# Optimization experiments

Hardware: AMD Instinct MI355X
Metric: run time of the kernel (lower is better)

Reference implementation:

```python
import jax, jax.numpy as jnp
import numpy as np

N_V, M, K, C, H, F, CO = 100000, 25000, 48, 64, 4, 256, 64


def setup_inputs() -> dict:
    key = jax.random.key(0)
    ks = jax.random.split(key, 16)
    w = lambda k, shape: (jax.random.normal(k, shape, jnp.float32) * 0.05)
    voxel_features = jax.random.normal(ks[0], (N_V, C), jnp.float32)
    voxel_coords = jax.random.uniform(ks[1], (N_V, 3), jnp.float32) * 70.0 - 35.0
    query_coords = jax.random.uniform(ks[2], (M, 3), jnp.float32) * 70.0 - 35.0
    key_indices = jax.random.randint(ks[3], (M, K), 0, N_V, jnp.int32)
    key_mask = jax.random.uniform(ks[4], (M, K)) < 0.3
    key_mask = key_mask.at[:, 0].set(False)  # guarantee >=1 valid key per query
    zeros = lambda n: jnp.zeros((n,), jnp.float32)
    ones = lambda n: jnp.ones((n,), jnp.float32)
    return dict(
        voxel_features=voxel_features, voxel_coords=voxel_coords,
        query_coords=query_coords, key_indices=key_indices, key_mask=key_mask,
        q_pos_w=w(ks[5], (C, 3)), q_pos_b=zeros(C),
        k_pos_w=w(ks[6], (C, 3)), k_pos_b=zeros(C),
        in_proj_w=w(ks[7], (3 * C, C)), in_proj_b=zeros(3 * C),
        out_proj_w=w(ks[8], (C, C)), out_proj_b=zeros(C),
        lin1_w=w(ks[9], (F, C)), lin1_b=zeros(F),
        lin2_w=w(ks[10], (C, F)), lin2_b=zeros(C),
        norm_g=ones(C), norm_b=zeros(C), norm_m=zeros(C), norm_v=ones(C),
        out_w=w(ks[11], (CO, C)), out_b=zeros(CO),
        bn2_g=ones(CO), bn2_b=zeros(CO), bn2_m=zeros(CO), bn2_v=ones(CO),
    )


def reference(voxel_features, voxel_coords, query_coords, key_indices, key_mask,
              q_pos_w, q_pos_b, k_pos_w, k_pos_b, in_proj_w, in_proj_b,
              out_proj_w, out_proj_b, lin1_w, lin1_b, lin2_w, lin2_b,
              norm_g, norm_b, norm_m, norm_v, out_w, out_b,
              bn2_g, bn2_b, bn2_m, bn2_v):
    m, k = key_indices.shape
    c = voxel_features.shape[1]
    h = H
    d = c // h
    # grouping_operation: gather per-query key features/coords  (M,K,C)/(M,K,3)
    key_feats = voxel_features[key_indices]
    rel = voxel_coords[key_indices] - query_coords[:, None, :]  # relative coords
    # k_pos_proj: Conv1d(3->C, kernel 1) + ReLU == pointwise linear
    key_pos = jax.nn.relu(jnp.einsum('mkt,ct->mkc', rel, k_pos_w) + k_pos_b)
    k_in = key_feats + key_pos                      # (M,K,C)
    # q_pos_proj: Linear(3->C) + ReLU
    q_in = jax.nn.relu(query_coords @ q_pos_w.T + q_pos_b)  # (M,C)
    # nn.MultiheadAttention, query len 1, batch = M, keys = K
    wq, wk, wv = jnp.split(in_proj_w, 3, axis=0)
    bq, bk, bv = jnp.split(in_proj_b, 3)
    q = ((q_in @ wq.T + bq) * (d ** -0.5)).reshape(m, h, d)
    kk = (k_in @ wk.T + bk).reshape(m, k, h, d)
    vv = (k_in @ wv.T + bv).reshape(m, k, h, d)
    s = jnp.einsum('mhd,mkhd->mhk', q, kk)
    s = jnp.where(key_mask[:, None, :], -1e9, s)    # key_padding_mask
    a = jax.nn.softmax(s, axis=-1)
    o = jnp.einsum('mhk,mkhd->mhd', a, vv).reshape(m, c)
    attend = o @ out_proj_w.T + out_proj_b          # (M,C)
    # FFN residual (dropouts are identity in eval)
    ff = jax.nn.relu(attend @ lin1_w.T + lin1_b) @ lin2_w.T + lin2_b
    x = attend + ff
    # BatchNorm1d (eval)
    x = (x - norm_m) / jnp.sqrt(norm_v + 1e-5) * norm_g + norm_b
    # output_layer: Linear -> BN -> ReLU
    y = x @ out_w.T + out_b
    y = (y - bn2_m) / jnp.sqrt(bn2_v + 1e-5) * bn2_g + bn2_b
    return jax.nn.relu(y)
```

## Files before the change

### kernel.cpp

```cpp
#include <hip/hip_runtime.h>
#include <math.h>

#define CC 64
#define KK 48
#define HH 4

typedef __attribute__((ext_vector_type(8))) short s16x8;
typedef __attribute__((ext_vector_type(4))) short s16x4;
typedef __attribute__((ext_vector_type(4))) float f32x4;

#define QW_OFF_U16 57344
#define CASTB 1024

#define WAVEFENCE() asm volatile("s_waitcnt lgkmcnt(0)" ::: "memory")

__device__ __forceinline__ unsigned short f2bf(float f) {
  return (unsigned short)((__float_as_uint(f) + 0x8000u) >> 16);
}
__device__ __forceinline__ float bf2f(unsigned short h) {
  return __uint_as_float(((unsigned)h) << 16);
}

__global__ __launch_bounds__(256) void setup_kernel(
    const float* __restrict__ ipw, const float* __restrict__ opw,
    const float* __restrict__ l1w, const float* __restrict__ l2w,
    const float* __restrict__ ow,
    const float* __restrict__ ng, const float* __restrict__ nb,
    const float* __restrict__ nm, const float* __restrict__ nv,
    const float* __restrict__ b2g, const float* __restrict__ b2b,
    const float* __restrict__ b2m, const float* __restrict__ b2v,
    const unsigned char* __restrict__ km,
    const float* __restrict__ vf, const float* __restrict__ vcoord,
    const float* __restrict__ qcoord, const float* __restrict__ qpw,
    const float* __restrict__ qpb, const float* __restrict__ ipb,
    float* __restrict__ ws,
    unsigned short* __restrict__ vfb, float4* __restrict__ vc4,
    unsigned short* __restrict__ qw_out, int M, int NV)
{
  unsigned short* wsu = (unsigned short*)ws;
  const int b = blockIdx.x;

  if (b < 210) {
    if (b == 209) {
      int any = 0;
      for (int i = threadIdx.x; i < 4096; i += 256)
        if ((i & 3) && km[i]) any = 1;
      __shared__ int sb;
      if (threadIdx.x == 0) sb = 0;
      __syncthreads();
      if (any) atomicOr(&sb, 1);
      __syncthreads();
      if (threadIdx.x == 0) ((int*)ws)[26880] = sb;
      return;
    }
    int e = b * 256 + threadIdx.x;
    if (e < 4096)        wsu[e] = f2bf(ipw[e]);
    else if (e < 8192)  { int i = e - 4096; int h = i >> 10, c = (i >> 4) & 63, d = i & 15;
                          wsu[e] = f2bf(ipw[(size_t)(64 + h * 16 + d) * 64 + c]); }
    else if (e < 12288)  wsu[e] = f2bf(ipw[e]);
    else if (e < 16384)  wsu[e] = f2bf(opw[e - 12288]);
    else if (e < 32768)  wsu[e] = f2bf(l1w[e - 16384]);
    else if (e < 49152)  wsu[e] = f2bf(l2w[e - 32768]);
    else if (e < 53248)  wsu[e] = f2bf(ow[e - 49152]);
    else if (e < 53312) { int c = e - 53248; float s = ng[c] / sqrtf(nv[c] + 1e-5f);
                          ws[26624 + c] = s; ws[26624 + 64 + c] = nb[c] - nm[c] * s; }
    else if (e < 53376) { int c = e - 53312; float s = b2g[c] / sqrtf(b2v[c] + 1e-5f);
                          ws[26752 + c] = s; ws[26752 + 64 + c] = b2b[c] - b2m[c] * s; }
    return;
  }

  if (b < 210 + CASTB) {
    const int i0 = (b - 210) * 256 + threadIdx.x;
    const int stride = CASTB * 256;
    for (int i = i0; i < NV * 16; i += stride) {
      const float4 v = *(const float4*)(vf + (size_t)i * 4);
      s16x4 p; p[0] = (short)f2bf(v.x); p[1] = (short)f2bf(v.y);
      p[2] = (short)f2bf(v.z); p[3] = (short)f2bf(v.w);
      *(s16x4*)(vfb + (size_t)i * 4) = p;
    }
    for (int i = i0; i < NV; i += stride)
      vc4[i] = make_float4(vcoord[i * 3], vcoord[i * 3 + 1], vcoord[i * 3 + 2], 0.f);
    return;
  }

  {
    __shared__ __align__(16) unsigned short xa[4][1024];
    __shared__ float qc[4][48];
    const int w = threadIdx.x >> 6, l = threadIdx.x & 63;
    const int col = l & 15, lg = l >> 4;
    const int r0 = (b - 210 - CASTB) * 64 + w * 16;

    if (l < 48) {
      int gi = r0 * 3 + l;
      qc[w][l] = (gi < M * 3) ? qcoord[gi] : 0.f;
    }
    const int c0 = col * 4;
    const float4 wA = *(const float4*)(qpw + c0 * 3);
    const float4 wB = *(const float4*)(qpw + c0 * 3 + 4);
    const float4 wC = *(const float4*)(qpw + c0 * 3 + 8);
    const float4 bq4 = *(const float4*)(qpb + c0);
    __syncthreads();

    #pragma unroll
    for (int i = 0; i < 4; ++i) {
      const int row = i * 4 + lg;
      const float x = qc[w][row * 3 + 0], y = qc[w][row * 3 + 1], z = qc[w][row * 3 + 2];
      s16x4 p;
      p[0] = (short)f2bf(fmaxf(wA.x * x + wA.y * y + wA.z * z + bq4.x, 0.f));
      p[1] = (short)f2bf(fmaxf(wA.w * x + wB.x * y + wB.y * z + bq4.y, 0.f));
      p[2] = (short)f2bf(fmaxf(wB.z * x + wB.w * y + wC.x * z + bq4.z, 0.f));
      p[3] = (short)f2bf(fmaxf(wC.y * x + wC.z * y + wC.w * z + bq4.w, 0.f));
      *(s16x4*)&xa[w][(row * 64 + c0) ^ ((row & 7) << 3)] = p;
    }
    __syncthreads();

    {
      s16x8 af0 = *(const s16x8*)&xa[w][(col * 64 + 0 + lg * 8) ^ ((col & 7) << 3)];
      s16x8 af1 = *(const s16x8*)&xa[w][(col * 64 + 32 + lg * 8) ^ ((col & 7) << 3)];
      f32x4 qv[4];
      #pragma unroll
      for (int nt = 0; nt < 4; ++nt) {
        f32x4 acc = {0.f, 0.f, 0.f, 0.f};
        #pragma unroll
        for (int kst = 0; kst < 2; ++kst) {
          const float* wr = ipw + (size_t)(nt * 16 + col) * 64 + kst * 32 + lg * 8;
          const float4 w0 = *(const float4*)wr;
          const float4 w1 = *(const float4*)(wr + 4);
          s16x8 bf;
          bf[0] = (short)f2bf(w0.x); bf[1] = (short)f2bf(w0.y);
          bf[2] = (short)f2bf(w0.z); bf[3] = (short)f2bf(w0.w);
          bf[4] = (short)f2bf(w1.x); bf[5] = (short)f2bf(w1.y);
          bf[6] = (short)f2bf(w1.z); bf[7] = (short)f2bf(w1.w);
          acc = __builtin_amdgcn_mfma_f32_16x16x32_bf16(kst == 0 ? af0 : af1, bf, acc, 0, 0, 0);
        }
        qv[nt] = acc;
      }
      __syncthreads();
      #pragma unroll
      for (int nt = 0; nt < 4; ++nt) {
        const int n = nt * 16 + col;
        const float bb = ipb[n];
        #pragma unroll
        for (int r = 0; r < 4; ++r) {
          const int row = lg * 4 + r;
          xa[w][(row * 64 + n) ^ ((row & 7) << 3)] = f2bf((qv[nt][r] + bb) * 0.25f);
        }
      }
    }
    __syncthreads();

    #pragma unroll
    for (int h = 0; h < HH; ++h) {
      s16x8 a = {0, 0, 0, 0, 0, 0, 0, 0};
      if (lg < 2)
        a = *(const s16x8*)&xa[w][(col * 64 + h * 16 + lg * 8) ^ ((col & 7) << 3)];
      #pragma unroll
      for (int nt = 0; nt < 4; ++nt) {
        const int n = nt * 16 + col;
        s16x8 bf = {0, 0, 0, 0, 0, 0, 0, 0};
        if (lg < 2) {
          #pragma unroll
          for (int j = 0; j < 8; ++j)
            ((unsigned short*)&bf)[j] = f2bf(ipw[(size_t)(64 + h * 16 + lg * 8 + j) * 64 + n]);
        }
        f32x4 acc = {0.f, 0.f, 0.f, 0.f};
        acc = __builtin_amdgcn_mfma_f32_16x16x32_bf16(a, bf, acc, 0, 0, 0);
        #pragma unroll
        for (int r = 0; r < 4; ++r) {
          const int m = lg * 4 + r;
          if (r0 + m < M)
            qw_out[(size_t)(r0 + m) * 256 + h * 64 + n] = f2bf(acc[r]);
        }
      }
    }
  }
}

__global__ __launch_bounds__(256, 4) void attn_hot(
    const unsigned short* __restrict__ vfb, const float4* __restrict__ vc4,
    const float* __restrict__ qcoord, const int* __restrict__ kidx,
    const unsigned char* __restrict__ km8, const int* __restrict__ km32,
    const int* __restrict__ maskfmt,
    const float* __restrict__ kpw, const float* __restrict__ kpb,
    const float* __restrict__ ipb,
    const unsigned short* __restrict__ wv_bf,
    const unsigned short* __restrict__ qw_pre,
    float* __restrict__ out, int M)
{
  __shared__ __align__(16) unsigned short shq[4][3456];
  __shared__ __align__(16) unsigned short wvl[4096];
  const int w = threadIdx.x >> 6, l = threadIdx.x & 63;
  const int col = l & 15, lg = l >> 4;
  int m = blockIdx.x * 4 + w;
  if (m >= M) m = M - 1;
  unsigned short* sh = shq[w];
  float* relf = (float*)(sh + 3072);
  const int is_u8 = *maskfmt;

  #pragma unroll
  for (int i = 0; i < 2; ++i) {
    const int ch = threadIdx.x * 2 + i;
    const int n = ch >> 3, g = ch & 7;
    const s16x8 v = *(const s16x8*)(wv_bf + n * 64 + g * 8);
    *(s16x8*)&wvl[n * 64 + ((g ^ (n & 7)) << 3)] = v;
  }

  const float qx = qcoord[m * 3 + 0], qy = qcoord[m * 3 + 1], qz = qcoord[m * 3 + 2];
  const int c0 = col * 4;
  const float4 kwA = *(const float4*)(kpw + c0 * 3);
  const float4 kwB = *(const float4*)(kpw + c0 * 3 + 4);
  const float4 kwC = *(const float4*)(kpw + c0 * 3 + 8);
  const float4 kbv = *(const float4*)(kpb + c0);

  const s16x8 qb0 = *(const s16x8*)(qw_pre + (size_t)m * 256 + (col & 3) * 64 + 0 + lg * 8);
  const s16x8 qb1 = *(const s16x8*)(qw_pre + (size_t)m * 256 + (col & 3) * 64 + 32 + lg * 8);

  unsigned char msk = 0;
  if (l < KK) {
    const int idx = kidx[m * KK + l];
    msk = is_u8 ? km8[m * KK + l] : (unsigned char)(km32[m * KK + l] != 0);
    const float4 vc = vc4[idx];
    float4 rr;
    rr.x = vc.x - qx; rr.y = vc.y - qy; rr.z = vc.z - qz;
    rr.w = __int_as_float(idx);
    *(float4*)(relf + l * 4) = rr;
  }
  const unsigned long long bm = __ballot(l < KK && msk);
  __syncthreads();

  #pragma unroll
  for (int half = 0; half < 2; ++half) {
    float4 ra[6]; s16x4 va[6];
    #pragma unroll
    for (int j = 0; j < 6; ++j) {
      const int k = half * 24 + j * 4 + lg;
      ra[j] = *(const float4*)(relf + k * 4);
      va[j] = *(const s16x4*)(vfb + (size_t)__float_as_int(ra[j].w) * 64 + c0);
    }
    #pragma unroll
    for (int j = 0; j < 6; ++j) {
      const int k = half * 24 + j * 4 + lg;
      const float p0 = fmaxf(kwA.x * ra[j].x + kwA.y * ra[j].y + kwA.z * ra[j].z + kbv.x, 0.f);
      const float p1 = fmaxf(kwA.w * ra[j].x + kwB.x * ra[j].y + kwB.y * ra[j].z + kbv.y, 0.f);
      const float p2 = fmaxf(kwB.z * ra[j].x + kwB.w * ra[j].y + kwC.x * ra[j].z + kbv.z, 0.f);
      const float p3 = fmaxf(kwC.y * ra[j].x + kwC.z * ra[j].y + kwC.w * ra[j].z + kbv.w, 0.f);
      s16x4 p;
      p[0] = (short)f2bf(bf2f((unsigned short)va[j][0]) + p0);
      p[1] = (short)f2bf(bf2f((unsigned short)va[j][1]) + p1);
      p[2] = (short)f2bf(bf2f((unsigned short)va[j][2]) + p2);
      p[3] = (short)f2bf(bf2f((unsigned short)va[j][3]) + p3);
      *(s16x4*)&sh[(k * 64 + c0) ^ ((k & 7) << 3)] = p;
    }
  }
  WAVEFENCE();

  s16x8 af[3][2];
  #pragma unroll
  for (int mt = 0; mt < 3; ++mt)
    #pragma unroll
    for (int kst = 0; kst < 2; ++kst) {
      const int row = mt * 16 + col;
      af[mt][kst] = *(const s16x8*)&sh[(row * 64 + kst * 32 + lg * 8) ^ ((row & 7) << 3)];
    }
  f32x4 sc[3];
  sc[0] = sc[1] = sc[2] = (f32x4){0.f, 0.f, 0.f, 0.f};
  __builtin_amdgcn_s_setprio(1);
  #pragma unroll
  for (int mt = 0; mt < 3; ++mt) {
    sc[mt] = __builtin_amdgcn_mfma_f32_16x16x32_bf16(af[mt][0], qb0, sc[mt], 0, 0, 0);
    sc[mt] = __builtin_amdgcn_mfma_f32_16x16x32_bf16(af[mt][1], qb1, sc[mt], 0, 0, 0);
  }
  __builtin_amdgcn_s_setprio(0);

  float sv[12];
  {
    float mx = -INFINITY;
    #pragma unroll
    for (int mt = 0; mt < 3; ++mt)
      #pragma unroll
      for (int r = 0; r < 4; ++r) {
        const int key = mt * 16 + lg * 4 + r;
        float v = sc[mt][r];
        if ((bm >> key) & 1ull) v = -1e30f;
        sv[mt * 4 + r] = v;
        mx = fmaxf(mx, v);
      }
    mx = fmaxf(mx, __shfl_xor(mx, 16, 64));
    mx = fmaxf(mx, __shfl_xor(mx, 32, 64));
    float sum = 0.f;
    #pragma unroll
    for (int i = 0; i < 12; ++i) { float e = __expf(sv[i] - mx); sv[i] = e; sum += e; }
    sum += __shfl_xor(sum, 16, 64);
    sum += __shfl_xor(sum, 32, 64);
    const float inv = 1.f / sum;
    #pragma unroll
    for (int i = 0; i < 12; ++i) sv[i] *= inv;
  }
  if (col < HH) {
    #pragma unroll
    for (int mt = 0; mt < 3; ++mt)
      #pragma unroll
      for (int r = 0; r < 4; ++r)
        relf[(mt * 16 + lg * 4 + r) * 4 + col] = sv[mt * 4 + r];
  }
  WAVEFENCE();

  f32x4 vva[4][3];
  __builtin_amdgcn_s_setprio(1);
  #pragma unroll
  for (int nt = 0; nt < 4; ++nt) {
    const int n = nt * 16 + col;
    vva[nt][0] = vva[nt][1] = vva[nt][2] = (f32x4){0.f, 0.f, 0.f, 0.f};
    #pragma unroll
    for (int kst = 0; kst < 2; ++kst) {
      const s16x8 b = *(const s16x8*)&wvl[(n * 64 + kst * 32 + lg * 8) ^ ((n & 7) << 3)];
      vva[nt][0] = __builtin_amdgcn_mfma_f32_16x16x32_bf16(af[0][kst], b, vva[nt][0], 0, 0, 0);
      vva[nt][1] = __builtin_amdgcn_mfma_f32_16x16x32_bf16(af[1][kst], b, vva[nt][1], 0, 0, 0);
      vva[nt][2] = __builtin_amdgcn_mfma_f32_16x16x32_bf16(af[2][kst], b, vva[nt][2], 0, 0, 0);
    }
  }
  __builtin_amdgcn_s_setprio(0);
  float op[4] = {0.f, 0.f, 0.f, 0.f};
  #pragma unroll
  for (int mt = 0; mt < 3; ++mt)
    #pragma unroll
    for (int r = 0; r < 4; ++r) {
      const float4 a4 = *(const float4*)(relf + (mt * 16 + lg * 4 + r) * 4);
      op[0] += a4.x * vva[0][mt][r];
      op[1] += a4.y * vva[1][mt][r];
      op[2] += a4.z * vva[2][mt][r];
      op[3] += a4.w * vva[3][mt][r];
    }
  #pragma unroll
  for (int nt = 0; nt < 4; ++nt) {
    op[nt] += __shfl_xor(op[nt], 16, 64);
    op[nt] += __shfl_xor(op[nt], 32, 64);
  }
  {
    float oo = (lg == 0) ? op[0] : (lg == 1) ? op[1] : (lg == 2) ? op[2] : op[3];
    oo += ipb[2 * CC + lg * 16 + col];
    out[(size_t)m * CC + lg * 16 + col] = oo;
  }
}

__global__ __launch_bounds__(256) void prep_kernel(
    const float* __restrict__ ipw, const float* __restrict__ opw,
    const float* __restrict__ l1w, const float* __restrict__ l2w,
    const float* __restrict__ ow,
    const float* __restrict__ ng, const float* __restrict__ nb,
    const float* __restrict__ nm, const float* __restrict__ nv,
    const float* __restrict__ b2g, const float* __restrict__ b2b,
    const float* __restrict__ b2m, const float* __restrict__ b2v,
    const unsigned char* __restrict__ km,
    float* __restrict__ ws)
{
  unsigned short* wsu = (unsigned short*)ws;
  if (blockIdx.x == 209) {
    int any = 0;
    for (int i = threadIdx.x; i < 4096; i += 256)
      if ((i & 3) && km[i]) any = 1;
    __shared__ int sb;
    if (threadIdx.x == 0) sb = 0;
    __syncthreads();
    if (any) atomicOr(&sb, 1);
    __syncthreads();
    if (threadIdx.x == 0) ((int*)ws)[26880] = sb;
    return;
  }
  int e = blockIdx.x * 256 + threadIdx.x;
  if (e < 4096)        wsu[e] = f2bf(ipw[e]);
  else if (e < 8192)  { int i = e - 4096; int h = i >> 10, c = (i >> 4) & 63, d = i & 15;
                        wsu[e] = f2bf(ipw[(size_t)(64 + h * 16 + d) * 64 + c]); }
  else if (e < 12288)  wsu[e] = f2bf(ipw[e]);
  else if (e < 16384)  wsu[e] = f2bf(opw[e - 12288]);
  else if (e < 32768)  wsu[e] = f2bf(l1w[e - 16384]);
  else if (e < 49152)  wsu[e] = f2bf(l2w[e - 32768]);
  else if (e < 53248)  wsu[e] = f2bf(ow[e - 49152]);
  else if (e < 53312) { int c = e - 53248; float s = ng[c] / sqrtf(nv[c] + 1e-5f);
                        ws[26624 + c] = s; ws[26624 + 64 + c] = nb[c] - nm[c] * s; }
  else if (e < 53376) { int c = e - 53312; float s = b2g[c] / sqrtf(b2v[c] + 1e-5f);
                        ws[26752 + c] = s; ws[26752 + 64 + c] = b2b[c] - b2m[c] * s; }
}

__global__ __launch_bounds__(256, 4) void attn_fallback(
    const float* __restrict__ vfeat, const float* __restrict__ vcoord,
    const float* __restrict__ qcoord, const int* __restrict__ kidx,
    const unsigned char* __restrict__ km8, const int* __restrict__ km32,
    const int* __restrict__ maskfmt,
    const float* __restrict__ qpw, const float* __restrict__ qpb,
    const float* __restrict__ kpw, const float* __restrict__ kpb,
    const float* __restrict__ ipb,
    const unsigned short* __restrict__ wq_bf,
    const unsigned short* __restrict__ wk2T_bf,
    const unsigned short* __restrict__ wv_bf,
    float* __restrict__ out, int M)
{
  __shared__ __align__(16) unsigned short shq[4][3776];
  __shared__ __align__(16) unsigned short wvl[4096];
  const int w = threadIdx.x >> 6, l = threadIdx.x & 63;
  const int col = l & 15, lg = l >> 4;
  int m = blockIdx.x * 4 + w;
  if (m >= M) m = M - 1;
  unsigned short* sh = shq[w];
  const int is_u8 = *maskfmt;
  float* relf = (float*)sh + 1696;

  #pragma unroll
  for (int i = 0; i < 2; ++i) {
    const int ch = threadIdx.x * 2 + i;
    const int n = ch >> 3, g = ch & 7;
    const s16x8 v = *(const s16x8*)(wv_bf + n * 64 + g * 8);
    *(s16x8*)&wvl[n * 64 + ((g ^ (n & 7)) << 3)] = v;
  }

  const float qx = qcoord[m * 3 + 0], qy = qcoord[m * 3 + 1], qz = qcoord[m * 3 + 2];
  const int c0 = col * 4;
  const float4 kwA = *(const float4*)(kpw + c0 * 3);
  const float4 kwB = *(const float4*)(kpw + c0 * 3 + 4);
  const float4 kwC = *(const float4*)(kpw + c0 * 3 + 8);
  const float4 kbv = *(const float4*)(kpb + c0);

  {
    float v = qpw[l * 3 + 0] * qx + qpw[l * 3 + 1] * qy + qpw[l * 3 + 2] * qz + qpb[l];
    sh[3328 + l] = f2bf(fmaxf(v, 0.f));
  }
  unsigned char msk = 0;
  if (l < KK) {
    int idx = kidx[m * KK + l];
    msk = is_u8 ? km8[m * KK + l] : (unsigned char)(km32[m * KK + l] != 0);
    relf[l * 4 + 0] = vcoord[idx * 3 + 0] - qx;
    relf[l * 4 + 1] = vcoord[idx * 3 + 1] - qy;
    relf[l * 4 + 2] = vcoord[idx * 3 + 2] - qz;
    relf[l * 4 + 3] = __int_as_float(idx);
  }
  const unsigned long long bm = __ballot(l < KK && msk);
  __syncthreads();

  {
    f32x4 qacc[4];
    #pragma unroll
    for (int nt = 0; nt < 4; ++nt) qacc[nt] = (f32x4){0.f, 0.f, 0.f, 0.f};
    #pragma unroll
    for (int kst = 0; kst < 2; ++kst) {
      const s16x8 a = *(const s16x8*)&sh[3328 + kst * 32 + lg * 8];
      #pragma unroll
      for (int nt = 0; nt < 4; ++nt) {
        const s16x8 b = *(const s16x8*)(wq_bf + (nt * 16 + col) * 64 + kst * 32 + lg * 8);
        qacc[nt] = __builtin_amdgcn_mfma_f32_16x16x32_bf16(a, b, qacc[nt], 0, 0, 0);
      }
    }
    __syncthreads();
    if (lg == 0) {
      #pragma unroll
      for (int nt = 0; nt < 4; ++nt)
        sh[3328 + nt * 16 + col] = f2bf((qacc[nt][0] + ipb[nt * 16 + col]) * 0.25f);
    }
    __syncthreads();
    f32x4 wacc[4];
    #pragma unroll
    for (int nt = 0; nt < 4; ++nt) wacc[nt] = (f32x4){0.f, 0.f, 0.f, 0.f};
    #pragma unroll
    for (int kst = 0; kst < 2; ++kst) {
      const int hblk = kst * 2 + (lg >> 1);
      s16x8 a = {0, 0, 0, 0, 0, 0, 0, 0};
      if (col == hblk) a = *(const s16x8*)&sh[3328 + kst * 32 + lg * 8];
      #pragma unroll
      for (int nt = 0; nt < 4; ++nt) {
        const s16x8 b = *(const s16x8*)(wk2T_bf + hblk * 1024 + (nt * 16 + col) * 16 + (lg & 1) * 8);
        wacc[nt] = __builtin_amdgcn_mfma_f32_16x16x32_bf16(a, b, wacc[nt], 0, 0, 0);
      }
    }
    if (lg == 0) {
      #pragma unroll
      for (int nt = 0; nt < 4; ++nt)
        #pragma unroll
        for (int r = 0; r < 4; ++r)
          sh[3072 + r * 64 + nt * 16 + col] = f2bf(wacc[nt][r]);
    }
  }

  #pragma unroll
  for (int half = 0; half < 2; ++half) {
    float4 ra[6], va[6];
    #pragma unroll
    for (int j = 0; j < 6; ++j) {
      const int k = half * 24 + j * 4 + lg;
      ra[j] = *(const float4*)(relf + k * 4);
      va[j] = *(const float4*)(vfeat + (size_t)__float_as_int(ra[j].w) * 64 + c0);
    }
    #pragma unroll
    for (int j = 0; j < 6; ++j) {
      const int k = half * 24 + j * 4 + lg;
      const float p0 = fmaxf(kwA.x * ra[j].x + kwA.y * ra[j].y + kwA.z * ra[j].z + kbv.x, 0.f);
      const float p1 = fmaxf(kwA.w * ra[j].x + kwB.x * ra[j].y + kwB.y * ra[j].z + kbv.y, 0.f);
// ... 104 lines not shown
  const unsigned short* l1_bf  = wsu + 16384;
  const unsigned short* l2_bf  = wsu + 32768;
  const unsigned short* ow_bf  = wsu + 49152;

  #pragma unroll
  for (int i = 0; i < 4; ++i) {
    int row = i * 4 + lg, cb = col * 4;
    float4 v = make_float4(0.f, 0.f, 0.f, 0.f);
    if (r0 + row < M) v = *(const float4*)(&inout[(size_t)(r0 + row) * 64 + cb]);
    s16x4 p; p[0] = (short)f2bf(v.x); p[1] = (short)f2bf(v.y);
    p[2] = (short)f2bf(v.z); p[3] = (short)f2bf(v.w);
    *(s16x4*)&XH[(row * 64 + cb) ^ ((row & 7) << 3)] = p;
  }

  s16x8 afa[2];
  #pragma unroll
  for (int kst = 0; kst < 2; ++kst)
    afa[kst] = *(const s16x8*)&XH[(col * 64 + kst * 32 + lg * 8) ^ ((col & 7) << 3)];
  f32x4 att[4];
  #pragma unroll
  for (int nt = 0; nt < 4; ++nt) {
    f32x4 acc = {0.f, 0.f, 0.f, 0.f};
    #pragma unroll
    for (int kst = 0; kst < 2; ++kst) {
      const s16x8 b = *(const s16x8*)&opw_bf[(nt * 16 + col) * 64 + kst * 32 + lg * 8];
      acc = __builtin_amdgcn_mfma_f32_16x16x32_bf16(afa[kst], b, acc, 0, 0, 0);
    }
    float bias = opb[nt * 16 + col];
    #pragma unroll
    for (int r = 0; r < 4; ++r) {
      acc[r] += bias;
      int row = lg * 4 + r;
      XB[(row * 64 + nt * 16 + col) ^ ((row & 7) << 3)] = (short)f2bf(acc[r]);
    }
    att[nt] = acc;
  }

  s16x8 afb[2];
  #pragma unroll
  for (int kst = 0; kst < 2; ++kst)
    afb[kst] = *(const s16x8*)&XB[(col * 64 + kst * 32 + lg * 8) ^ ((col & 7) << 3)];
  #pragma unroll
  for (int nt = 0; nt < 16; ++nt) {
    f32x4 acc = {0.f, 0.f, 0.f, 0.f};
    #pragma unroll
    for (int kst = 0; kst < 2; ++kst) {
      const s16x8 b = *(const s16x8*)&l1_bf[(nt * 16 + col) * 64 + kst * 32 + lg * 8];
      acc = __builtin_amdgcn_mfma_f32_16x16x32_bf16(afb[kst], b, acc, 0, 0, 0);
    }
    float bias = l1b[nt * 16 + col];
    #pragma unroll
    for (int r = 0; r < 4; ++r) {
      float h = fmaxf(acc[r] + bias, 0.f);
      int row = lg * 4 + r;
      XH[(row * 256 + nt * 16 + col) ^ ((row & 7) << 3)] = (short)f2bf(h);
    }
  }

  s16x8 afh[8];
  #pragma unroll
  for (int kst = 0; kst < 8; ++kst)
    afh[kst] = *(const s16x8*)&XH[(col * 256 + kst * 32 + lg * 8) ^ ((col & 7) << 3)];
  #pragma unroll
  for (int nt = 0; nt < 4; ++nt) {
    f32x4 acc = {0.f, 0.f, 0.f, 0.f};
    #pragma unroll
    for (int kst = 0; kst < 8; ++kst) {
      const s16x8 b = *(const s16x8*)&l2_bf[(nt * 16 + col) * 256 + kst * 32 + lg * 8];
      acc = __builtin_amdgcn_mfma_f32_16x16x32_bf16(afh[kst], b, acc, 0, 0, 0);
    }
    int nc = nt * 16 + col;
    float bias = l2b[nc], sN = nrm[nc], tN = nrm[64 + nc];
    #pragma unroll
    for (int r = 0; r < 4; ++r) {
      float x = (att[nt][r] + acc[r] + bias) * sN + tN;
      int row = lg * 4 + r;
      XB[(row * 64 + nc) ^ ((row & 7) << 3)] = (short)f2bf(x);
    }
  }

  s16x8 afx[2];
  #pragma unroll
  for (int kst = 0; kst < 2; ++kst)
    afx[kst] = *(const s16x8*)&XB[(col * 64 + kst * 32 + lg * 8) ^ ((col & 7) << 3)];
  #pragma unroll
  for (int nt = 0; nt < 4; ++nt) {
    f32x4 acc = {0.f, 0.f, 0.f, 0.f};
    #pragma unroll
    for (int kst = 0; kst < 2; ++kst) {
      const s16x8 b = *(const s16x8*)&ow_bf[(nt * 16 + col) * 64 + kst * 32 + lg * 8];
      acc = __builtin_amdgcn_mfma_f32_16x16x32_bf16(afx[kst], b, acc, 0, 0, 0);
    }
    int nc = nt * 16 + col;
    float bias = ob[nc], sB = bn2[nc], tB = bn2[64 + nc];
    #pragma unroll
    for (int r = 0; r < 4; ++r) {
      float y = fmaxf((acc[r] + bias) * sB + tB, 0.f);
      int row = lg * 4 + r;
      if (r0 + row < M) inout[(size_t)(r0 + row) * 64 + nc] = y;
    }
  }
}

extern "C" void kernel_launch(void* const* d_in, const int* in_sizes, int n_in,
                              void* d_out, int out_size, void* d_ws, size_t ws_size,
                              hipStream_t stream) {
  const float* vfeat  = (const float*)d_in[0];
  const float* vcoord = (const float*)d_in[1];
  const float* qcoord = (const float*)d_in[2];
  const int*   kidx   = (const int*)d_in[3];
  const unsigned char* km8  = (const unsigned char*)d_in[4];
  const int*           km32 = (const int*)d_in[4];
  const float* qpw = (const float*)d_in[5];
  const float* qpb = (const float*)d_in[6];
  const float* kpw = (const float*)d_in[7];
  const float* kpb = (const float*)d_in[8];
  const float* ipw = (const float*)d_in[9];
  const float* ipb = (const float*)d_in[10];
  const float* opw = (const float*)d_in[11];
  const float* opb = (const float*)d_in[12];
  const float* l1w = (const float*)d_in[13];
  const float* l1b = (const float*)d_in[14];
  const float* l2w = (const float*)d_in[15];
  const float* l2b = (const float*)d_in[16];
  const float* ng  = (const float*)d_in[17];
  const float* nb  = (const float*)d_in[18];
  const float* nm  = (const float*)d_in[19];
  const float* nv  = (const float*)d_in[20];
  const float* ow  = (const float*)d_in[21];
  const float* ob  = (const float*)d_in[22];
  const float* b2g = (const float*)d_in[23];
  const float* b2b = (const float*)d_in[24];
  const float* b2m = (const float*)d_in[25];
  const float* b2v = (const float*)d_in[26];

  const int M  = in_sizes[2] / 3;
  const int NV = in_sizes[0] / 64;
  float* ws  = (float*)d_ws;
  float* out = (float*)d_out;
  unsigned short* wsu = (unsigned short*)ws;
  const int* flag = (const int*)ws + 26880;

  const size_t need = (size_t)114688 + (size_t)M * 512 + (size_t)NV * 128 + (size_t)NV * 16;
  const int hot = (ws_size >= need) ? 1 : 0;
  unsigned short* qw  = wsu + QW_OFF_U16;
  unsigned short* vfb = wsu + QW_OFF_U16 + (size_t)M * 256;
  float4* vc4 = (float4*)(wsu + QW_OFF_U16 + (size_t)M * 256 + (size_t)NV * 64);

  if (hot) {
    const int qblocks = (M + 63) / 64;
    setup_kernel<<<210 + CASTB + qblocks, 256, 0, stream>>>(
        ipw, opw, l1w, l2w, ow, ng, nb, nm, nv, b2g, b2b, b2m, b2v, km8,
        vfeat, vcoord, qcoord, qpw, qpb, ipb, ws, vfb, vc4, qw, M, NV);
    attn_hot<<<(M + 3) / 4, 256, 0, stream>>>(vfb, vc4, qcoord, kidx,
                                              km8, km32, flag, kpw, kpb, ipb,
                                              wsu + 8192, qw, out, M);
  } else {
    prep_kernel<<<210, 256, 0, stream>>>(ipw, opw, l1w, l2w, ow,
                                         ng, nb, nm, nv, b2g, b2b, b2m, b2v, km8, ws);
    attn_fallback<<<(M + 3) / 4, 256, 0, stream>>>(vfeat, vcoord, qcoord, kidx,
                                                   km8, km32, flag,
                                                   qpw, qpb, kpw, kpb, ipb,
                                                   wsu, wsu + 4096, wsu + 8192, out, M);
  }
  chain_kernel<<<(M + 63) / 64, 256, 0, stream>>>(out, wsu, opb, l1b, l2b, ob,
                                                  ws + 26624, ws + 26752, M);
}
```

Baseline: 93.80 us.

## Fuse attention with output projection, FFN and BN chain in one kernel

The attention kernel now processes 16 queries per block (4 per wave, looped) and then runs the out-projection, FFN, residual, batchnorm and output layer on those 16 rows in shared memory using MFMA. This removes the separate chain kernel launch and the fp32 round trip of the attention output through global memory. The setup kernel also stages the Wq and transposed Wk weights into LDS as bf16 once per block instead of converting them from global memory per lane. The costs are fewer blocks with serialized per-query work, extra block-wide barriers, and bf16 rounding of intermediate activations.

```diff
diff --git a/kernel.cpp b/kernel.cpp
--- a/kernel.cpp
+++ b/kernel.cpp
@@ -84,12 +84,19 @@
   }
 
   {
+    __shared__ __align__(16) unsigned short wql[4096];
+    __shared__ __align__(16) unsigned short wkTl[4096];
     __shared__ __align__(16) unsigned short xa[4][1024];
     __shared__ float qc[4][48];
     const int w = threadIdx.x >> 6, l = threadIdx.x & 63;
     const int col = l & 15, lg = l >> 4;
     const int r0 = (b - 210 - CASTB) * 64 + w * 16;
 
+    for (int i = threadIdx.x; i < 4096; i += 256) {
+      const int r = i >> 6, d = i & 63;
+      wql[i ^ ((r & 7) << 3)] = f2bf(ipw[i]);
+      wkTl[(d * 64 + r) ^ ((d & 7) << 3)] = f2bf(ipw[4096 + i]);
+    }
     if (l < 48) {
       int gi = r0 * 3 + l;
       qc[w][l] = (gi < M * 3) ? qcoord[gi] : 0.f;
@@ -120,19 +127,12 @@
       f32x4 qv[4];
       #pragma unroll
       for (int nt = 0; nt < 4; ++nt) {
+        const int n = nt * 16 + col;
         f32x4 acc = {0.f, 0.f, 0.f, 0.f};
-        #pragma unroll
-        for (int kst = 0; kst < 2; ++kst) {
-          const float* wr = ipw + (size_t)(nt * 16 + col) * 64 + kst * 32 + lg * 8;
-          const float4 w0 = *(const float4*)wr;
-          const float4 w1 = *(const float4*)(wr + 4);
-          s16x8 bf;
-          bf[0] = (short)f2bf(w0.x); bf[1] = (short)f2bf(w0.y);
-          bf[2] = (short)f2bf(w0.z); bf[3] = (short)f2bf(w0.w);
-          bf[4] = (short)f2bf(w1.x); bf[5] = (short)f2bf(w1.y);
-          bf[6] = (short)f2bf(w1.z); bf[7] = (short)f2bf(w1.w);
-          acc = __builtin_amdgcn_mfma_f32_16x16x32_bf16(kst == 0 ? af0 : af1, bf, acc, 0, 0, 0);
-        }
+        acc = __builtin_amdgcn_mfma_f32_16x16x32_bf16(af0,
+                *(const s16x8*)&wql[(n * 64 + 0 + lg * 8) ^ ((col & 7) << 3)], acc, 0, 0, 0);
+        acc = __builtin_amdgcn_mfma_f32_16x16x32_bf16(af1,
+                *(const s16x8*)&wql[(n * 64 + 32 + lg * 8) ^ ((col & 7) << 3)], acc, 0, 0, 0);
         qv[nt] = acc;
       }
       __syncthreads();
@@ -158,11 +158,8 @@
       for (int nt = 0; nt < 4; ++nt) {
         const int n = nt * 16 + col;
         s16x8 bf = {0, 0, 0, 0, 0, 0, 0, 0};
-        if (lg < 2) {
-          #pragma unroll
-          for (int j = 0; j < 8; ++j)
-            ((unsigned short*)&bf)[j] = f2bf(ipw[(size_t)(64 + h * 16 + lg * 8 + j) * 64 + n]);
-        }
+        if (lg < 2)
+          bf = *(const s16x8*)&wkTl[(n * 64 + h * 16 + lg * 8) ^ ((col & 7) << 3)];
         f32x4 acc = {0.f, 0.f, 0.f, 0.f};
         acc = __builtin_amdgcn_mfma_f32_16x16x32_bf16(a, bf, acc, 0, 0, 0);
         #pragma unroll
@@ -176,7 +173,7 @@
   }
 }
 
-__global__ __launch_bounds__(256, 4) void attn_hot(
+__global__ __launch_bounds__(256, 4) void attn_mega(
     const unsigned short* __restrict__ vfb, const float4* __restrict__ vc4,
     const float* __restrict__ qcoord, const int* __restrict__ kidx,
     const unsigned char* __restrict__ km8, const int* __restrict__ km32,
@@ -185,16 +182,21 @@
     const float* __restrict__ ipb,
     const unsigned short* __restrict__ wv_bf,
     const unsigned short* __restrict__ qw_pre,
+    const unsigned short* __restrict__ wsu,
+    const float* __restrict__ opb, const float* __restrict__ l1b,
+    const float* __restrict__ l2b, const float* __restrict__ ob,
+    const float* __restrict__ nrm, const float* __restrict__ bn2,
     float* __restrict__ out, int M)
 {
-  __shared__ __align__(16) unsigned short shq[4][3456];
-  __shared__ __align__(16) unsigned short wvl[4096];
+  __shared__ __align__(16) unsigned short L[18944];
   const int w = threadIdx.x >> 6, l = threadIdx.x & 63;
   const int col = l & 15, lg = l >> 4;
-  int m = blockIdx.x * 4 + w;
-  if (m >= M) m = M - 1;
-  unsigned short* sh = shq[w];
+  unsigned short* wvl = L;
+  unsigned short* sh  = L + 4096 + w * 3456;
   float* relf = (float*)(sh + 3072);
+  unsigned short* XA = L + 17920;
+  unsigned short* XH = L + 4096;
+  unsigned short* XB = L + 8192;
   const int is_u8 = *maskfmt;
 
   #pragma unroll
@@ -205,141 +207,248 @@
     *(s16x8*)&wvl[n * 64 + ((g ^ (n & 7)) << 3)] = v;
   }
 
-  const float qx = qcoord[m * 3 + 0], qy = qcoord[m * 3 + 1], qz = qcoord[m * 3 + 2];
   const int c0 = col * 4;
   const float4 kwA = *(const float4*)(kpw + c0 * 3);
   const float4 kwB = *(const float4*)(kpw + c0 * 3 + 4);
   const float4 kwC = *(const float4*)(kpw + c0 * 3 + 8);
   const float4 kbv = *(const float4*)(kpb + c0);
-
-  const s16x8 qb0 = *(const s16x8*)(qw_pre + (size_t)m * 256 + (col & 3) * 64 + 0 + lg * 8);
-  const s16x8 qb1 = *(const s16x8*)(qw_pre + (size_t)m * 256 + (col & 3) * 64 + 32 + lg * 8);
-
-  unsigned char msk = 0;
-  if (l < KK) {
-    const int idx = kidx[m * KK + l];
-    msk = is_u8 ? km8[m * KK + l] : (unsigned char)(km32[m * KK + l] != 0);
-    const float4 vc = vc4[idx];
-    float4 rr;
-    rr.x = vc.x - qx; rr.y = vc.y - qy; rr.z = vc.z - qz;
-    rr.w = __int_as_float(idx);
-    *(float4*)(relf + l * 4) = rr;
-  }
-  const unsigned long long bm = __ballot(l < KK && msk);
+  const float bv = ipb[2 * CC + lg * 16 + col];
   __syncthreads();
 
-  #pragma unroll
-  for (int half = 0; half < 2; ++half) {
-    float4 ra[6]; s16x4 va[6];
-    #pragma unroll
-    for (int j = 0; j < 6; ++j) {
-      const int k = half * 24 + j * 4 + lg;
-      ra[j] = *(const float4*)(relf + k * 4);
-      va[j] = *(const s16x4*)(vfb + (size_t)__float_as_int(ra[j].w) * 64 + c0);
-    }
-    #pragma unroll
-    for (int j = 0; j < 6; ++j) {
-      const int k = half * 24 + j * 4 + lg;
-      const float p0 = fmaxf(kwA.x * ra[j].x + kwA.y * ra[j].y + kwA.z * ra[j].z + kbv.x, 0.f);
-      const float p1 = fmaxf(kwA.w * ra[j].x + kwB.x * ra[j].y + kwB.y * ra[j].z + kbv.y, 0.f);
-      const float p2 = fmaxf(kwB.z * ra[j].x + kwB.w * ra[j].y + kwC.x * ra[j].z + kbv.z, 0.f);
-      const float p3 = fmaxf(kwC.y * ra[j].x + kwC.z * ra[j].y + kwC.w * ra[j].z + kbv.w, 0.f);
-      s16x4 p;
-      p[0] = (short)f2bf(bf2f((unsigned short)va[j][0]) + p0);
-      p[1] = (short)f2bf(bf2f((unsigned short)va[j][1]) + p1);
-      p[2] = (short)f2bf(bf2f((unsigned short)va[j][2]) + p2);
-      p[3] = (short)f2bf(bf2f((unsigned short)va[j][3]) + p3);
-      *(s16x4*)&sh[(k * 64 + c0) ^ ((k & 7) << 3)] = p;
-    }
-  }
-  WAVEFENCE();
-
-  s16x8 af[3][2];
-  #pragma unroll
-  for (int mt = 0; mt < 3; ++mt)
+  #pragma unroll 1
+  for (int qi = 0; qi < 4; ++qi) {
+    int m = blockIdx.x * 16 + w * 4 + qi;
+    if (m >= M) m = M - 1;
+    WAVEFENCE();
+
+    const float qx = qcoord[m * 3 + 0], qy = qcoord[m * 3 + 1], qz = qcoord[m * 3 + 2];
+    const s16x8 qb0 = *(const s16x8*)(qw_pre + (size_t)m * 256 + (col & 3) * 64 + 0 + lg * 8);
+    const s16x8 qb1 = *(const s16x8*)(qw_pre + (size_t)m * 256 + (col & 3) * 64 + 32 + lg * 8);
+
+    unsigned char msk = 0;
+    if (l < KK) {
+      const int idx = kidx[m * KK + l];
+      msk = is_u8 ? km8[m * KK + l] : (unsigned char)(km32[m * KK + l] != 0);
+      const float4 vc = vc4[idx];
+      float4 rr;
+      rr.x = vc.x - qx; rr.y = vc.y - qy; rr.z = vc.z - qz;
+      rr.w = __int_as_float(idx);
+      *(float4*)(relf + l * 4) = rr;
+    }
+    const unsigned long long bm = __ballot(l < KK && msk);
+    WAVEFENCE();
+
+    #pragma unroll
+    for (int half = 0; half < 2; ++half) {
+      float4 ra[6]; s16x4 va[6];
+      #pragma unroll
+      for (int j = 0; j < 6; ++j) {
+        const int k = half * 24 + j * 4 + lg;
+        ra[j] = *(const float4*)(relf + k * 4);
+        va[j] = *(const s16x4*)(vfb + (size_t)__float_as_int(ra[j].w) * 64 + c0);
+      }
+      #pragma unroll
+      for (int j = 0; j < 6; ++j) {
+        const int k = half * 24 + j * 4 + lg;
+        const float p0 = fmaxf(kwA.x * ra[j].x + kwA.y * ra[j].y + kwA.z * ra[j].z + kbv.x, 0.f);
+        const float p1 = fmaxf(kwA.w * ra[j].x + kwB.x * ra[j].y + kwB.y * ra[j].z + kbv.y, 0.f);
+        const float p2 = fmaxf(kwB.z * ra[j].x + kwB.w * ra[j].y + kwC.x * ra[j].z + kbv.z, 0.f);
+        const float p3 = fmaxf(kwC.y * ra[j].x + kwC.z * ra[j].y + kwC.w * ra[j].z + kbv.w, 0.f);
+        s16x4 p;
+        p[0] = (short)f2bf(bf2f((unsigned short)va[j][0]) + p0);
+        p[1] = (short)f2bf(bf2f((unsigned short)va[j][1]) + p1);
+        p[2] = (short)f2bf(bf2f((unsigned short)va[j][2]) + p2);
+        p[3] = (short)f2bf(bf2f((unsigned short)va[j][3]) + p3);
+        *(s16x4*)&sh[(k * 64 + c0) ^ ((k & 7) << 3)] = p;
+      }
+    }
+    WAVEFENCE();
+
+    s16x8 af[3][2];
+    #pragma unroll
+    for (int mt = 0; mt < 3; ++mt)
+      #pragma unroll
+      for (int kst = 0; kst < 2; ++kst) {
+        const int row = mt * 16 + col;
+        af[mt][kst] = *(const s16x8*)&sh[(row * 64 + kst * 32 + lg * 8) ^ ((row & 7) << 3)];
+      }
+    f32x4 sc[3];
+    sc[0] = sc[1] = sc[2] = (f32x4){0.f, 0.f, 0.f, 0.f};
+    __builtin_amdgcn_s_setprio(1);
+    #pragma unroll
+    for (int mt = 0; mt < 3; ++mt) {
+      sc[mt] = __builtin_amdgcn_mfma_f32_16x16x32_bf16(af[mt][0], qb0, sc[mt], 0, 0, 0);
+      sc[mt] = __builtin_amdgcn_mfma_f32_16x16x32_bf16(af[mt][1], qb1, sc[mt], 0, 0, 0);
+    }
+    __builtin_amdgcn_s_setprio(0);
+
+    float sv[12];
+    {
+      float mx = -INFINITY;
+      #pragma unroll
+      for (int mt = 0; mt < 3; ++mt)
+        #pragma unroll
+        for (int r = 0; r < 4; ++r) {
+          const int key = mt * 16 + lg * 4 + r;
+          float v = sc[mt][r];
+          if ((bm >> key) & 1ull) v = -1e30f;
+          sv[mt * 4 + r] = v;
+          mx = fmaxf(mx, v);
+        }
+      mx = fmaxf(mx, __shfl_xor(mx, 16, 64));
+      mx = fmaxf(mx, __shfl_xor(mx, 32, 64));
+      float sum = 0.f;
+      #pragma unroll
+      for (int i = 0; i < 12; ++i) { float e = __expf(sv[i] - mx); sv[i] = e; sum += e; }
+      sum += __shfl_xor(sum, 16, 64);
+      sum += __shfl_xor(sum, 32, 64);
+      const float inv = 1.f / sum;
+      #pragma unroll
+      for (int i = 0; i < 12; ++i) sv[i] *= inv;
+    }
+    if (col < HH) {
+      #pragma unroll
+      for (int mt = 0; mt < 3; ++mt)
+        #pragma unroll
+        for (int r = 0; r < 4; ++r)
+          relf[(mt * 16 + lg * 4 + r) * 4 + col] = sv[mt * 4 + r];
+    }
+    WAVEFENCE();
+
+    f32x4 vva[4][3];
+    __builtin_amdgcn_s_setprio(1);
+    #pragma unroll
+    for (int nt = 0; nt < 4; ++nt) {
+      const int n = nt * 16 + col;
+      vva[nt][0] = vva[nt][1] = vva[nt][2] = (f32x4){0.f, 0.f, 0.f, 0.f};
+      #pragma unroll
+      for (int kst = 0; kst < 2; ++kst) {
+        const s16x8 bb = *(const s16x8*)&wvl[(n * 64 + kst * 32 + lg * 8) ^ ((n & 7) << 3)];
+        vva[nt][0] = __builtin_amdgcn_mfma_f32_16x16x32_bf16(af[0][kst], bb, vva[nt][0], 0, 0, 0);
+        vva[nt][1] = __builtin_amdgcn_mfma_f32_16x16x32_bf16(af[1][kst], bb, vva[nt][1], 0, 0, 0);
+        vva[nt][2] = __builtin_amdgcn_mfma_f32_16x16x32_bf16(af[2][kst], bb, vva[nt][2], 0, 0, 0);
+      }
+    }
+    __builtin_amdgcn_s_setprio(0);
+    float op[4] = {0.f, 0.f, 0.f, 0.f};
+    #pragma unroll
+    for (int mt = 0; mt < 3; ++mt)
+      #pragma unroll
+      for (int r = 0; r < 4; ++r) {
+        const float4 a4 = *(const float4*)(relf + (mt * 16 + lg * 4 + r) * 4);
+        op[0] += a4.x * vva[0][mt][r];
+        op[1] += a4.y * vva[1][mt][r];
+        op[2] += a4.z * vva[2][mt][r];
+        op[3] += a4.w * vva[3][mt][r];
+      }
+    #pragma unroll
+    for (int nt = 0; nt < 4; ++nt) {
+      op[nt] += __shfl_xor(op[nt], 16, 64);
+      op[nt] += __shfl_xor(op[nt], 32, 64);
+    }
+    {
+      float oo = (lg == 0) ? op[0] : (lg == 1) ? op[1] : (lg == 2) ? op[2] : op[3];
+      oo += bv;
+      const int row = w * 4 + qi;
+      XA[(row * 64 + lg * 16 + col) ^ ((row & 7) << 3)] = f2bf(oo);
+    }
+  }
+  __syncthreads();
+
+  const unsigned short* opw_bf = wsu + 12288;
+  const unsigned short* l1_bf  = wsu + 16384;
+  const unsigned short* l2_bf  = wsu + 32768;
+  const unsigned short* ow_bf  = wsu + 49152;
+
+  s16x8 afa[2];
+  #pragma unroll
+  for (int kst = 0; kst < 2; ++kst)
+    afa[kst] = *(const s16x8*)&XA[(col * 64 + kst * 32 + lg * 8) ^ ((col & 7) << 3)];
+  f32x4 att;
+  {
+    f32x4 acc = {0.f, 0.f, 0.f, 0.f};
     #pragma unroll
     for (int kst = 0; kst < 2; ++kst) {
-      const int row = mt * 16 + col;
-      af[mt][kst] = *(const s16x8*)&sh[(row * 64 + kst * 32 + lg * 8) ^ ((row & 7) << 3)];
-    }
-  f32x4 sc[3];
-  sc[0] = sc[1] = sc[2] = (f32x4){0.f, 0.f, 0.f, 0.f};
-  __builtin_amdgcn_s_setprio(1);
-  #pragma unroll
-  for (int mt = 0; mt < 3; ++mt) {
-    sc[mt] = __builtin_amdgcn_mfma_f32_16x16x32_bf16(af[mt][0], qb0, sc[mt], 0, 0, 0);
-    sc[mt] = __builtin_amdgcn_mfma_f32_16x16x32_bf16(af[mt][1], qb1, sc[mt], 0, 0, 0);
-  }
-  __builtin_amdgcn_s_setprio(0);
-
-  float sv[12];
+      const s16x8 bb = *(const s16x8*)&opw_bf[(w * 16 + col) * 64 + kst * 32 + lg * 8];
+      acc = __builtin_amdgcn_mfma_f32_16x16x32_bf16(afa[kst], bb, acc, 0, 0, 0);
+    }
+    const float bias = opb[w * 16 + col];
+    #pragma unroll
+    for (int r = 0; r < 4; ++r) {
+      acc[r] += bias;
+      const int row = lg * 4 + r;
+      XB[(row * 64 + w * 16 + col) ^ ((row & 7) << 3)] = (short)f2bf(acc[r]);
+    }
+    att = acc;
+  }
+  __syncthreads();
+
   {
-    float mx = -INFINITY;
-    #pragma unroll
-    for (int mt = 0; mt < 3; ++mt)
+    s16x8 afb[2];
+    #pragma unroll
+    for (int kst = 0; kst < 2; ++kst)
+      afb[kst] = *(const s16x8*)&XB[(col * 64 + kst * 32 + lg * 8) ^ ((col & 7) << 3)];
+    #pragma unroll
+    for (int nt2 = 0; nt2 < 4; ++nt2) {
+      const int ntg = w * 4 + nt2;
+      f32x4 acc = {0.f, 0.f, 0.f, 0.f};
+      #pragma unroll
+      for (int kst = 0; kst < 2; ++kst) {
+        const s16x8 bb = *(const s16x8*)&l1_bf[(ntg * 16 + col) * 64 + kst * 32 + lg * 8];
+        acc = __builtin_amdgcn_mfma_f32_16x16x32_bf16(afb[kst], bb, acc, 0, 0, 0);
+      }
+      const float bias = l1b[ntg * 16 + col];
       #pragma unroll
       for (int r = 0; r < 4; ++r) {
-        const int key = mt * 16 + lg * 4 + r;
-        float v = sc[mt][r];
-        if ((bm >> key) & 1ull) v = -1e30f;
-        sv[mt * 4 + r] = v;
-        mx = fmaxf(mx, v);
-      }
-    mx = fmaxf(mx, __shfl_xor(mx, 16, 64));
-    mx = fmaxf(mx, __shfl_xor(mx, 32, 64));
-    float sum = 0.f;
-    #pragma unroll
-    for (int i = 0; i < 12; ++i) { float e = __expf(sv[i] - mx); sv[i] = e; sum += e; }
-    sum += __shfl_xor(sum, 16, 64);
-    sum += __shfl_xor(sum, 32, 64);
-    const float inv = 1.f / sum;
-    #pragma unroll
-    for (int i = 0; i < 12; ++i) sv[i] *= inv;
-  }
-  if (col < HH) {
-    #pragma unroll
-    for (int mt = 0; mt < 3; ++mt)
-      #pragma unroll
-      for (int r = 0; r < 4; ++r)
-        relf[(mt * 16 + lg * 4 + r) * 4 + col] = sv[mt * 4 + r];
-  }
-  WAVEFENCE();
-
-  f32x4 vva[4][3];
-  __builtin_amdgcn_s_setprio(1);
-  #pragma unroll
-  for (int nt = 0; nt < 4; ++nt) {
-    const int n = nt * 16 + col;
-    vva[nt][0] = vva[nt][1] = vva[nt][2] = (f32x4){0.f, 0.f, 0.f, 0.f};
+        const float h = fmaxf(acc[r] + bias, 0.f);
+        const int row = lg * 4 + r;
+        XH[(row * 256 + ntg * 16 + col) ^ ((row & 7) << 3)] = (short)f2bf(h);
+      }
+    }
+  }
+  __syncthreads();
+
+  {
+    s16x8 afh[8];
+    #pragma unroll
+    for (int kst = 0; kst < 8; ++kst)
+      afh[kst] = *(const s16x8*)&XH[(col * 256 + kst * 32 + lg * 8) ^ ((col & 7) << 3)];
+    f32x4 acc = {0.f, 0.f, 0.f, 0.f};
+    #pragma unroll
+    for (int kst = 0; kst < 8; ++kst) {
+      const s16x8 bb = *(const s16x8*)&l2_bf[(w * 16 + col) * 256 + kst * 32 + lg * 8];
+      acc = __builtin_amdgcn_mfma_f32_16x16x32_bf16(afh[kst], bb, acc, 0, 0, 0);
+    }
+    const int nc = w * 16 + col;
+    const float bias = l2b[nc], sN = nrm[nc], tN = nrm[64 + nc];
+    #pragma unroll
+    for (int r = 0; r < 4; ++r) {
+      const float x = (att[r] + acc[r] + bias) * sN + tN;
+      const int row = lg * 4 + r;
+      XB[(row * 64 + nc) ^ ((row & 7) << 3)] = (short)f2bf(x);
+    }
+  }
+  __syncthreads();
+
+  {
+    s16x8 afx[2];
+    #pragma unroll
+    for (int kst = 0; kst < 2; ++kst)
+      afx[kst] = *(const s16x8*)&XB[(col * 64 + kst * 32 + lg * 8) ^ ((col & 7) << 3)];
+    f32x4 acc = {0.f, 0.f, 0.f, 0.f};
     #pragma unroll
     for (int kst = 0; kst < 2; ++kst) {
-      const s16x8 b = *(const s16x8*)&wvl[(n * 64 + kst * 32 + lg * 8) ^ ((n & 7) << 3)];
-      vva[nt][0] = __builtin_amdgcn_mfma_f32_16x16x32_bf16(af[0][kst], b, vva[nt][0], 0, 0, 0);
-      vva[nt][1] = __builtin_amdgcn_mfma_f32_16x16x32_bf16(af[1][kst], b, vva[nt][1], 0, 0, 0);
-      vva[nt][2] = __builtin_amdgcn_mfma_f32_16x16x32_bf16(af[2][kst], b, vva[nt][2], 0, 0, 0);
-    }
-  }
-  __builtin_amdgcn_s_setprio(0);
-  float op[4] = {0.f, 0.f, 0.f, 0.f};
-  #pragma unroll
-  for (int mt = 0; mt < 3; ++mt)
+      const s16x8 bb = *(const s16x8*)&ow_bf[(w * 16 + col) * 64 + kst * 32 + lg * 8];
+      acc = __builtin_amdgcn_mfma_f32_16x16x32_bf16(afx[kst], bb, acc, 0, 0, 0);
+    }
+    const int nc = w * 16 + col;
+    const float bias = ob[nc], sB = bn2[nc], tB = bn2[64 + nc];
     #pragma unroll
     for (int r = 0; r < 4; ++r) {
-      const float4 a4 = *(const float4*)(relf + (mt * 16 + lg * 4 + r) * 4);
-      op[0] += a4.x * vva[0][mt][r];
-      op[1] += a4.y * vva[1][mt][r];
-      op[2] += a4.z * vva[2][mt][r];
-      op[3] += a4.w * vva[3][mt][r];
-    }
-  #pragma unroll
-  for (int nt = 0; nt < 4; ++nt) {
-    op[nt] += __shfl_xor(op[nt], 16, 64);
-    op[nt] += __shfl_xor(op[nt], 32, 64);
-  }
-  {
-    float oo = (lg == 0) ? op[0] : (lg == 1) ? op[1] : (lg == 2) ? op[2] : op[3];
-    oo += ipb[2 * CC + lg * 16 + col];
-    out[(size_t)m * CC + lg * 16 + col] = oo;
+      const float y = fmaxf((acc[r] + bias) * sB + tB, 0.f);
+      const int q = blockIdx.x * 16 + lg * 4 + r;
+      if (q < M) out[(size_t)q * 64 + nc] = y;
+    }
   }
 }
 
@@ -750,9 +859,10 @@
     setup_kernel<<<210 + CASTB + qblocks, 256, 0, stream>>>(
         ipw, opw, l1w, l2w, ow, ng, nb, nm, nv, b2g, b2b, b2m, b2v, km8,
         vfeat, vcoord, qcoord, qpw, qpb, ipb, ws, vfb, vc4, qw, M, NV);
-    attn_hot<<<(M + 3) / 4, 256, 0, stream>>>(vfb, vc4, qcoord, kidx,
-                                              km8, km32, flag, kpw, kpb, ipb,
-                                              wsu + 8192, qw, out, M);
+    attn_mega<<<(M + 15) / 16, 256, 0, stream>>>(
+        vfb, vc4, qcoord, kidx, km8, km32, flag, kpw, kpb, ipb,
+        wsu + 8192, qw, wsu, opb, l1b, l2b, ob,
+        ws + 26624, ws + 26752, out, M);
   } else {
     prep_kernel<<<210, 256, 0, stream>>>(ipw, opw, l1w, l2w, ow,
                                          ng, nb, nm, nv, b2g, b2b, b2m, b2v, km8, ws);
@@ -760,7 +870,7 @@
                                                    km8, km32, flag,
                                                    qpw, qpb, kpw, kpb, ipb,
                                                    wsu, wsu + 4096, wsu + 8192, out, M);
-  }
-  chain_kernel<<<(M + 63) / 64, 256, 0, stream>>>(out, wsu, opb, l1b, l2b, ob,
-                                                  ws + 26624, ws + 26752, M);
+    chain_kernel<<<(M + 63) / 64, 256, 0, stream>>>(out, wsu, opb, l1b, l2b, ob,
+                                                    ws + 26624, ws + 26752, M);
+  }
 }
```

Measured after the change: 152.9 us. 1.63x slower.

## Stage Wq/Wk in LDS for query projection; keep Wv in registers in attention

Applied to the files above, without the earlier changes.

In the query-projection part of the setup kernel, Wq and a transposed Wk are converted to bf16 once per block into swizzled LDS tiles. This replaces per-MFMA global loads and fp32-to-bf16 conversions, including strided scalar loads for Wk. In the hot attention kernel, the shared Wv tile is replaced by per-lane register fragments loaded straight from global memory, and the block-wide __syncthreads becomes a wave-level LDS fence. This removes a block barrier and LDS traffic but adds 32 VGPRs under a 4-wave occupancy bound, which may cause spills.

```diff
diff --git a/kernel.cpp b/kernel.cpp
--- a/kernel.cpp
+++ b/kernel.cpp
@@ -84,12 +84,19 @@
   }
 
   {
+    __shared__ __align__(16) unsigned short wql[4096];
+    __shared__ __align__(16) unsigned short wkTl[4096];
     __shared__ __align__(16) unsigned short xa[4][1024];
     __shared__ float qc[4][48];
     const int w = threadIdx.x >> 6, l = threadIdx.x & 63;
     const int col = l & 15, lg = l >> 4;
     const int r0 = (b - 210 - CASTB) * 64 + w * 16;
 
+    for (int i = threadIdx.x; i < 4096; i += 256) {
+      const int r = i >> 6, d = i & 63;
+      wql[i ^ ((r & 7) << 3)] = f2bf(ipw[i]);
+      wkTl[(d * 64 + r) ^ ((d & 7) << 3)] = f2bf(ipw[4096 + i]);
+    }
     if (l < 48) {
       int gi = r0 * 3 + l;
       qc[w][l] = (gi < M * 3) ? qcoord[gi] : 0.f;
@@ -120,19 +127,12 @@
       f32x4 qv[4];
       #pragma unroll
       for (int nt = 0; nt < 4; ++nt) {
+        const int n = nt * 16 + col;
         f32x4 acc = {0.f, 0.f, 0.f, 0.f};
-        #pragma unroll
-        for (int kst = 0; kst < 2; ++kst) {
-          const float* wr = ipw + (size_t)(nt * 16 + col) * 64 + kst * 32 + lg * 8;
-          const float4 w0 = *(const float4*)wr;
-          const float4 w1 = *(const float4*)(wr + 4);
-          s16x8 bf;
-          bf[0] = (short)f2bf(w0.x); bf[1] = (short)f2bf(w0.y);
-          bf[2] = (short)f2bf(w0.z); bf[3] = (short)f2bf(w0.w);
-          bf[4] = (short)f2bf(w1.x); bf[5] = (short)f2bf(w1.y);
-          bf[6] = (short)f2bf(w1.z); bf[7] = (short)f2bf(w1.w);
-          acc = __builtin_amdgcn_mfma_f32_16x16x32_bf16(kst == 0 ? af0 : af1, bf, acc, 0, 0, 0);
-        }
+        acc = __builtin_amdgcn_mfma_f32_16x16x32_bf16(af0,
+                *(const s16x8*)&wql[(n * 64 + 0 + lg * 8) ^ ((col & 7) << 3)], acc, 0, 0, 0);
+        acc = __builtin_amdgcn_mfma_f32_16x16x32_bf16(af1,
+                *(const s16x8*)&wql[(n * 64 + 32 + lg * 8) ^ ((col & 7) << 3)], acc, 0, 0, 0);
         qv[nt] = acc;
       }
       __syncthreads();
@@ -158,11 +158,8 @@
       for (int nt = 0; nt < 4; ++nt) {
         const int n = nt * 16 + col;
         s16x8 bf = {0, 0, 0, 0, 0, 0, 0, 0};
-        if (lg < 2) {
-          #pragma unroll
-          for (int j = 0; j < 8; ++j)
-            ((unsigned short*)&bf)[j] = f2bf(ipw[(size_t)(64 + h * 16 + lg * 8 + j) * 64 + n]);
-        }
+        if (lg < 2)
+          bf = *(const s16x8*)&wkTl[(n * 64 + h * 16 + lg * 8) ^ ((col & 7) << 3)];
         f32x4 acc = {0.f, 0.f, 0.f, 0.f};
         acc = __builtin_amdgcn_mfma_f32_16x16x32_bf16(a, bf, acc, 0, 0, 0);
         #pragma unroll
@@ -188,7 +185,6 @@
     float* __restrict__ out, int M)
 {
   __shared__ __align__(16) unsigned short shq[4][3456];
-  __shared__ __align__(16) unsigned short wvl[4096];
   const int w = threadIdx.x >> 6, l = threadIdx.x & 63;
   const int col = l & 15, lg = l >> 4;
   int m = blockIdx.x * 4 + w;
@@ -197,13 +193,12 @@
   float* relf = (float*)(sh + 3072);
   const int is_u8 = *maskfmt;
 
-  #pragma unroll
-  for (int i = 0; i < 2; ++i) {
-    const int ch = threadIdx.x * 2 + i;
-    const int n = ch >> 3, g = ch & 7;
-    const s16x8 v = *(const s16x8*)(wv_bf + n * 64 + g * 8);
-    *(s16x8*)&wvl[n * 64 + ((g ^ (n & 7)) << 3)] = v;
-  }
+  s16x8 wvb[4][2];
+  #pragma unroll
+  for (int nt = 0; nt < 4; ++nt)
+    #pragma unroll
+    for (int kst = 0; kst < 2; ++kst)
+      wvb[nt][kst] = *(const s16x8*)(wv_bf + (size_t)(nt * 16 + col) * 64 + kst * 32 + lg * 8);
 
   const float qx = qcoord[m * 3 + 0], qy = qcoord[m * 3 + 1], qz = qcoord[m * 3 + 2];
   const int c0 = col * 4;
@@ -226,7 +221,7 @@
     *(float4*)(relf + l * 4) = rr;
   }
   const unsigned long long bm = __ballot(l < KK && msk);
-  __syncthreads();
+  WAVEFENCE();
 
   #pragma unroll
   for (int half = 0; half < 2; ++half) {
@@ -309,14 +304,12 @@
   __builtin_amdgcn_s_setprio(1);
   #pragma unroll
   for (int nt = 0; nt < 4; ++nt) {
-    const int n = nt * 16 + col;
     vva[nt][0] = vva[nt][1] = vva[nt][2] = (f32x4){0.f, 0.f, 0.f, 0.f};
     #pragma unroll
     for (int kst = 0; kst < 2; ++kst) {
-      const s16x8 b = *(const s16x8*)&wvl[(n * 64 + kst * 32 + lg * 8) ^ ((n & 7) << 3)];
-      vva[nt][0] = __builtin_amdgcn_mfma_f32_16x16x32_bf16(af[0][kst], b, vva[nt][0], 0, 0, 0);
-      vva[nt][1] = __builtin_amdgcn_mfma_f32_16x16x32_bf16(af[1][kst], b, vva[nt][1], 0, 0, 0);
-      vva[nt][2] = __builtin_amdgcn_mfma_f32_16x16x32_bf16(af[2][kst], b, vva[nt][2], 0, 0, 0);
+      vva[nt][0] = __builtin_amdgcn_mfma_f32_16x16x32_bf16(af[0][kst], wvb[nt][kst], vva[nt][0], 0, 0, 0);
+      vva[nt][1] = __builtin_amdgcn_mfma_f32_16x16x32_bf16(af[1][kst], wvb[nt][kst], vva[nt][1], 0, 0, 0);
+      vva[nt][2] = __builtin_amdgcn_mfma_f32_16x16x32_bf16(af[2][kst], wvb[nt][kst], vva[nt][2], 0, 0, 0);
     }
   }
   __builtin_amdgcn_s_setprio(0);
```

After: 95.91 us. +2.2%, slower.
